# Kernel optimization log

Hardware: AMD Instinct MI355X
Metric: run time of the kernel (lower is better)

The kernel has to match this reference:

```python
import jax, jax.numpy as jnp
import numpy as np

K = 128      # knowledge_n (= net1 = prednet output width)
LOW = 64     # low_dim
PP = 64      # pp_dim
STU = 50000  # student_n
EXER = 20000 # exer_n
S_RANGES = [(0, 9999), (10000, 19999)]
NR = len(S_RANGES)
B = 4096


def setup_inputs() -> dict:
    key = jax.random.key(0)
    ks = jax.random.split(key, 16)

    def xavier(k, shape):
        fan_in, fan_out = shape[-1], shape[-2] if len(shape) > 1 else shape[-1]
        lim = np.sqrt(6.0 / (fan_in + fan_out))
        return jax.random.uniform(k, shape, jnp.float32, -lim, lim)

    return {
        "stu_id": jax.random.randint(ks[0], (B,), 0, STU),
        "exer_id": jax.random.randint(ks[1], (B,), 0, EXER),
        "kn_emb": jnp.ones((B, K), jnp.float32),
        "student_emb": xavier(ks[2], (NR, STU, LOW)),          # ParameterList stacked
        "prompt_stu": xavier(ks[3], (STU, PP)),
        "knowledge_emb": jax.random.normal(ks[4], (K, LOW), jnp.float32),
        "k_difficulty": xavier(ks[5], (EXER, LOW)),
        "s_exer_vectors": jax.random.uniform(ks[6], (NR, PP), jnp.float32),
        "W1": xavier(ks[7], (K, K + LOW)),                      # prednet_full1 (no bias)
        "W2": xavier(ks[8], (K, K + LOW)),                      # prednet_full2 (no bias)
        "W3": xavier(ks[9], (1, K)),                            # prednet_full3
        "b3": jnp.zeros((1,), jnp.float32),
        "fc1_W": xavier(ks[10], (K, PP + K)),
        "fc1_b": jnp.zeros((K,), jnp.float32),
        "fc2_W": xavier(ks[11], (K, PP + K)),
        "fc2_b": jnp.zeros((K,), jnp.float32),
    }


def reference(stu_id, exer_id, kn_emb, student_emb, prompt_stu, knowledge_emb,
              k_difficulty, s_exer_vectors, W1, W2, W3, b3, fc1_W, fc1_b, fc2_W, fc2_b):
    sig = jax.nn.sigmoid
    kle = knowledge_emb  # [K, LOW]

    # --- student side ---
    # prompt_stu.repeat(NR, 1) then index_select == index prompt_stu with stu_id % STU
    p_stu = prompt_stu[stu_id % STU]                              # [B, PP]
    stu_cat = student_emb.reshape(NR * STU, LOW)                  # concat of ParameterList
    old_stu = sig(stu_cat[stu_id] @ kle.T)                        # [B, K]
    stu_e = sig(jnp.concatenate([p_stu, old_stu], 1) @ fc1_W.T + fc1_b)  # [B, K]

    # --- exercise side ---
    counts = np.array([r[1] - r[0] + 1 for r in S_RANGES])
    temp_vectors = jnp.repeat(s_exer_vectors, counts, axis=0, total_repeat_length=EXER)
    p_exer = sig(temp_vectors[exer_id])                           # [B, PP]
    old_exer = sig(sig(k_difficulty[exer_id]) @ kle.T)            # [B, K]
    exer_e = sig(jnp.concatenate([p_exer, old_exer], 1) @ fc2_W.T + fc2_b)  # [B, K]

    # --- per-concept interaction ---
    # cat([x_broadcast, kn_vector], 2) @ W.T splits into x @ Wa.T + kle @ Wb.T
    W1a, W1b = W1[:, :K], W1[:, K:]
    W2a, W2b = W2[:, :K], W2[:, K:]
    preference = sig((stu_e @ W1a.T)[:, None, :] + (kle @ W1b.T)[None, :, :])   # [B, K, K]
    diff = sig((exer_e @ W2a.T)[:, None, :] + (kle @ W2b.T)[None, :, :])        # [B, K, K]

    o = sig((preference - diff) @ W3.T + b3)                      # [B, K, 1]
    sum_out = jnp.sum(o * kn_emb[:, :, None], axis=1)             # [B, 1]
    count = jnp.sum(kn_emb, axis=1, keepdims=True)
    return sum_out / count
```

## Files before the change

### kernel.cpp

```cpp
#include <hip/hip_runtime.h>
#include <hip/hip_bf16.h>

#define STUN   50000
#define BATCH  4096
#define LOG2E  1.4426950408889634f

__device__ __forceinline__ float fexp2(float x){ return __builtin_amdgcn_exp2f(x); }
__device__ __forceinline__ float frcp (float x){ return __builtin_amdgcn_rcpf(x); }
__device__ __forceinline__ float fsig (float x){ return frcp(1.0f + fexp2(-LOG2E * x)); }

__global__ __launch_bounds__(128) void k_pre(
    const float* __restrict__ kle,
    const float* __restrict__ W1,
    const float* __restrict__ W2,
    const float* __restrict__ fc1_W,
    const float* __restrict__ fc2_W,
    float* __restrict__ kle4,
    float* __restrict__ fc1i,
    float* __restrict__ fc2i,
    float* __restrict__ W1ai,
    float* __restrict__ W2ai,
    float* __restrict__ A1i,
    float* __restrict__ A2i)
{
    const int bid = blockIdx.x;
    const int t   = threadIdx.x;
    if (bid < 16) {
        const int u4 = bid;
        float4 v;
        v.x = kle[t * 64 + u4 * 4 + 0];
        v.y = kle[t * 64 + u4 * 4 + 1];
        v.z = kle[t * 64 + u4 * 4 + 2];
        v.w = kle[t * 64 + u4 * 4 + 3];
        *(float4*)&kle4[(u4 * 128 + t) * 4] = v;
    } else if (bid < 64) {
        const int u4 = bid - 16;
        float4 v;
        v.x = fc1_W[t * 192 + u4 * 4 + 0];
        v.y = fc1_W[t * 192 + u4 * 4 + 1];
        v.z = fc1_W[t * 192 + u4 * 4 + 2];
        v.w = fc1_W[t * 192 + u4 * 4 + 3];
        *(float4*)&fc1i[(u4 * 128 + t) * 4] = v;
    } else if (bid < 112) {
        const int u4 = bid - 64;
        float4 v;
        v.x = fc2_W[t * 192 + u4 * 4 + 0];
        v.y = fc2_W[t * 192 + u4 * 4 + 1];
        v.z = fc2_W[t * 192 + u4 * 4 + 2];
        v.w = fc2_W[t * 192 + u4 * 4 + 3];
        *(float4*)&fc2i[(u4 * 128 + t) * 4] = v;
    } else if (bid < 144) {
        const int u4 = bid - 112;
        float4 v;
        v.x = W1[t * 192 + u4 * 4 + 0];
        v.y = W1[t * 192 + u4 * 4 + 1];
        v.z = W1[t * 192 + u4 * 4 + 2];
        v.w = W1[t * 192 + u4 * 4 + 3];
        *(float4*)&W1ai[(u4 * 128 + t) * 4] = v;
    } else if (bid < 176) {
        const int u4 = bid - 144;
        float4 v;
        v.x = W2[t * 192 + u4 * 4 + 0];
        v.y = W2[t * 192 + u4 * 4 + 1];
        v.z = W2[t * 192 + u4 * 4 + 2];
        v.w = W2[t * 192 + u4 * 4 + 3];
        *(float4*)&W2ai[(u4 * 128 + t) * 4] = v;
    } else if (bid < 304) {
        const int j = bid - 176;
        float acc = 0.f;
        #pragma unroll
        for (int u4 = 0; u4 < 16; ++u4) {
            const float4 kv = *(const float4*)&kle[t * 64 + u4 * 4];
            const float4 wv = *(const float4*)&W1[j * 192 + 128 + u4 * 4];
            acc += kv.x * wv.x + kv.y * wv.y + kv.z * wv.z + kv.w * wv.w;
        }
        A1i[((j >> 2) * 128 + t) * 4 + (j & 3)] = -LOG2E * acc;
    } else {
        const int j = bid - 304;
        float acc = 0.f;
        #pragma unroll
        for (int u4 = 0; u4 < 16; ++u4) {
            const float4 kv = *(const float4*)&kle[t * 64 + u4 * 4];
            const float4 wv = *(const float4*)&W2[j * 192 + 128 + u4 * 4];
            acc += kv.x * wv.x + kv.y * wv.y + kv.z * wv.z + kv.w * wv.w;
        }
        A2i[((j >> 2) * 128 + t) * 4 + (j & 3)] = -LOG2E * acc;
    }
}

__global__ __launch_bounds__(512, 4) void k_fused(
    const int*   __restrict__ stu_id,
    const int*   __restrict__ exer_id,
    const float* __restrict__ student_emb,
    const float* __restrict__ prompt_stu,
    const float* __restrict__ k_diff,
    const float* __restrict__ s_exer,
    const float* __restrict__ kle4,
    const float* __restrict__ fc1i,
    const float* __restrict__ fc2i,
    const float* __restrict__ W1ai,
    const float* __restrict__ W2ai,
    const float* __restrict__ fc1_b,
    const float* __restrict__ fc2_b,
    const float* __restrict__ A1i,
    const float* __restrict__ A2i,
    const float* __restrict__ W3,
    const float* __restrict__ b3,
    const float* __restrict__ kn,
    float* __restrict__ out)
{
    __shared__ __align__(16) float sh_in [4][64][8];
    __shared__ __align__(16) float sh_old[2][128][8];
    __shared__ __align__(16) float sh_e  [2][128][8];
    __shared__ __align__(16) float sh_s  [2][8][128];
    __shared__ __align__(16) float ps    [2][8][128];
    __shared__ float sW3[128];
    __shared__ __align__(16) float red[8][64][4];
    __shared__ float red2_o[2][2][4];
    __shared__ float red2_k[2][2][4];

    const int t  = threadIdx.x;
    const int b0 = blockIdx.x * 8;

    {
        const int g   = t >> 6;
        const int u   = t & 63;
        const int sid = stu_id[b0 + g];
        const int eid = exer_id[b0 + g];
        const int er  = (eid >= 10000) ? 1 : 0;
        sh_in[0][u][g] = student_emb[sid * 64 + u];
        sh_in[1][u][g] = fsig(k_diff[eid * 64 + u]);
        sh_in[2][u][g] = prompt_stu[(sid % STUN) * 64 + u];
        sh_in[3][u][g] = fsig(s_exer[er * 64 + u]);
    }
    if (t < 32) *(float4*)&sW3[t * 4] = *(const float4*)&W3[t * 4];
    __syncthreads();

    const int ug   = t >> 8;
    const int tt   = t & 255;
    const int half = tt >> 7;
    const int idx  = tt & 127;

    float acc[8];

#define FMA8(xbase) { \
        const float4 x0 = *(const float4*)&(xbase)[0]; \
        const float4 x1 = *(const float4*)&(xbase)[4]; \
        acc[0] += wv * x0.x; acc[1] += wv * x0.y; acc[2] += wv * x0.z; acc[3] += wv * x0.w; \
        acc[4] += wv * x1.x; acc[5] += wv * x1.y; acc[6] += wv * x1.z; acc[7] += wv * x1.w; }

#define WSTEP(WARR, XARR, u4) { \
        const float4 w4 = *(const float4*)&WARR[((u4) * 128 + idx) * 4]; \
        { const float wv = w4.x; FMA8(XARR[(u4)*4+0]); } \
        { const float wv = w4.y; FMA8(XARR[(u4)*4+1]); } \
        { const float wv = w4.z; FMA8(XARR[(u4)*4+2]); } \
        { const float wv = w4.w; FMA8(XARR[(u4)*4+3]); } }

#define WSTEPO(WARR, XARR, u4, uoff) { \
        const float4 w4 = *(const float4*)&WARR[((u4) * 128 + idx) * 4]; \
        { const float wv = w4.x; FMA8(XARR[((u4)-(uoff))*4+0]); } \
        { const float wv = w4.y; FMA8(XARR[((u4)-(uoff))*4+1]); } \
        { const float wv = w4.z; FMA8(XARR[((u4)-(uoff))*4+2]); } \
        { const float wv = w4.w; FMA8(XARR[((u4)-(uoff))*4+3]); } }

    #pragma unroll
    for (int b = 0; b < 8; ++b) acc[b] = 0.f;
    {
        const int u4a = ug * 8;
        #pragma unroll 4
        for (int u4 = u4a; u4 < u4a + 8; ++u4) WSTEP(kle4, sh_in[half], u4);
    }
    if (ug == 1) {
        #pragma unroll
        for (int b = 0; b < 8; ++b) ps[half][b][idx] = acc[b];
    }
    __syncthreads();
    if (ug == 0) {
        #pragma unroll
        for (int b = 0; b < 8; ++b)
            sh_old[half][idx][b] = fsig(acc[b] + ps[half][b][idx]);
    }
    __syncthreads();

    #pragma unroll
    for (int b = 0; b < 8; ++b) acc[b] = 0.f;
    {
        const float* fcT = half ? fc2i : fc1i;
        if (ug == 0) {
            #pragma unroll 4
            for (int u4 = 0; u4 < 16; ++u4) WSTEP(fcT, sh_in[2 + half], u4);
            #pragma unroll 4
            for (int u4 = 16; u4 < 24; ++u4) WSTEPO(fcT, sh_old[half], u4, 16);
        } else {
            #pragma unroll 4
            for (int u4 = 24; u4 < 48; ++u4) WSTEPO(fcT, sh_old[half], u4, 16);
        }
    }
    if (ug == 1) {
        #pragma unroll
        for (int b = 0; b < 8; ++b) ps[half][b][idx] = acc[b];
    }
    __syncthreads();
    if (ug == 0) {
        const float bias = (half ? fc2_b : fc1_b)[idx];
        #pragma unroll
        for (int b = 0; b < 8; ++b)
            sh_e[half][idx][b] = fsig(acc[b] + ps[half][b][idx] + bias);
    }
    __syncthreads();

    #pragma unroll
    for (int b = 0; b < 8; ++b) acc[b] = 0.f;
    {
        const float* WT = half ? W2ai : W1ai;
        const int u4a = ug * 16;
        #pragma unroll 4
        for (int u4 = u4a; u4 < u4a + 16; ++u4) WSTEP(WT, sh_e[half], u4);
    }
    if (ug == 1) {
        #pragma unroll
        for (int b = 0; b < 8; ++b) ps[half][b][idx] = acc[b];
    }
    __syncthreads();
    if (ug == 0) {
        #pragma unroll
        for (int b = 0; b < 8; ++b)
            sh_s[half][b][idx] = -LOG2E * (acc[b] + ps[half][b][idx]);
    }
#undef FMA8
#undef WSTEP
#undef WSTEPO
    __syncthreads();

    const int w   = t >> 6;
    const int kk  = t & 63;
    const int jh  = w >> 2;
    const int kh  = (w >> 1) & 1;
    const int bq  = w & 1;
    const int k2  = kk + kh * 64;
    const int ib  = bq * 4;

    const float4* A1v = (const float4*)A1i + (jh * 16) * 128 + k2;
    const float4* A2v = (const float4*)A2i + (jh * 16) * 128 + k2;

    float ac0 = 0.f, ac1 = 0.f, ac2 = 0.f, ac3 = 0.f;

    #pragma unroll 2
    for (int j4 = 0; j4 < 16; ++j4) {
        const int j = jh * 64 + j4 * 4;
        const float4 a1 = A1v[j4 * 128];
        const float4 a2 = A2v[j4 * 128];
        const float4 w3 = *(const float4*)&sW3[j];

#define SIGPAIR(acc, s1, s2, a1c, a2c, wv) { \
        const float uu = fexp2((s1) + (a1c)); \
        const float vv = fexp2((s2) + (a2c)); \
        const float dd = frcp((1.f + uu) * (1.f + vv)); \
        acc += ((vv - uu) * dd) * (wv); }

#define BODY(acc, bi) { \
        const float4 s1 = *(const float4*)&sh_s[0][ib + bi][j]; \
        const float4 s2 = *(const float4*)&sh_s[1][ib + bi][j]; \
        SIGPAIR(acc, s1.x, s2.x, a1.x, a2.x, w3.x); \
        SIGPAIR(acc, s1.y, s2.y, a1.y, a2.y, w3.y); \
        SIGPAIR(acc, s1.z, s2.z, a1.z, a2.z, w3.z); \
        SIGPAIR(acc, s1.w, s2.w, a1.w, a2.w, w3.w); }

        BODY(ac0, 0);
        BODY(ac1, 1);
        BODY(ac2, 2);
        BODY(ac3, 3);
#undef BODY
#undef SIGPAIR
    }

    red[w][kk][0] = ac0; red[w][kk][1] = ac1;
    red[w][kk][2] = ac2; red[w][kk][3] = ac3;
    __syncthreads();
    if (w < 4) {
        const float bb3 = b3[0];
        const float4 other = *(const float4*)&red[w + 4][kk][0];
        float to[4] = { ac0 + other.x, ac1 + other.y, ac2 + other.z, ac3 + other.w };
        float co[4], ck[4];
        #pragma unroll
        for (int i = 0; i < 4; ++i) {
            const float o   = fsig(to[i] + bb3);
            const float knv = kn[(b0 + ib + i) * 128 + k2];
            co[i] = o * knv;
            ck[i] = knv;
        }
        #pragma unroll
        for (int off = 1; off < 64; off <<= 1) {
            #pragma unroll
            for (int i = 0; i < 4; ++i) {
                co[i] += __shfl_xor(co[i], off);
                ck[i] += __shfl_xor(ck[i], off);
            }
        }
        if (kk == 0) {
            #pragma unroll
            for (int i = 0; i < 4; ++i) {
                red2_o[kh][bq][i] = co[i];
                red2_k[kh][bq][i] = ck[i];
            }
        }
    }
    __syncthreads();
    if (t < 8) {
        const int b  = t;
        const int q  = b >> 2;
        const int i  = b & 3;
        const float so = red2_o[0][q][i] + red2_o[1][q][i];
        const float sk = red2_k[0][q][i] + red2_k[1][q][i];
        out[b0 + b] = so / sk;
    }
}

extern "C" void kernel_launch(void* const* d_in, const int* in_sizes, int n_in,
                              void* d_out, int out_size, void* d_ws, size_t ws_size,
                              hipStream_t stream)
{
    const int*   stu_id      = (const int*)  d_in[0];
    const int*   exer_id     = (const int*)  d_in[1];
    const float* kn_emb      = (const float*)d_in[2];
    const float* student_emb = (const float*)d_in[3];
    const float* prompt_stu  = (const float*)d_in[4];
    const float* kle         = (const float*)d_in[5];
    const float* k_diff      = (const float*)d_in[6];
    const float* s_exer      = (const float*)d_in[7];
    const float* W1          = (const float*)d_in[8];
    const float* W2          = (const float*)d_in[9];
    const float* W3          = (const float*)d_in[10];
    const float* b3          = (const float*)d_in[11];
    const float* fc1_W       = (const float*)d_in[12];
    const float* fc1_b       = (const float*)d_in[13];
    const float* fc2_W       = (const float*)d_in[14];
    const float* fc2_b       = (const float*)d_in[15];
    float* out = (float*)d_out;

    float* ws   = (float*)d_ws;
    float* kle4 = ws;
    float* fc1i = kle4 + 8192;
    float* fc2i = fc1i + 24576;
    float* W1ai = fc2i + 24576;
    float* W2ai = W1ai + 16384;
    float* A1i  = W2ai + 16384;
    float* A2i  = A1i  + 16384;

    k_pre<<<432, 128, 0, stream>>>(kle, W1, W2, fc1_W, fc2_W,
                                   kle4, fc1i, fc2i, W1ai, W2ai, A1i, A2i);
    k_fused<<<BATCH / 8, 512, 0, stream>>>(stu_id, exer_id, student_emb, prompt_stu,
                                           k_diff, s_exer, kle4, fc1i, fc2i,
                                           W1ai, W2ai, fc1_b, fc2_b,
                                           A1i, A2i, W3, b3, kn_emb, out);
}
```

Measured before the change: 53.89 us.

## Factor exp2 into precomputed exponentials and split fused kernel into prep and main

Uses exp(a+b)=exp(a)*exp(b) to precompute exponentials of the per-concept terms and of the per-sample projections, so the B×K×K inner loop needs multiplies and one reciprocal instead of two exp2 calls per element. The fused kernel is split into a prep kernel that writes per-sample exponentials to a workspace and a main kernel over 2 samples per block with 256 threads. This adds a global round trip and an extra launch, and the product form may overflow to inf for large pre-activations. The fp32 product could lose accuracy in extreme cases.

```diff
diff --git a/kernel.cpp b/kernel.cpp
--- a/kernel.cpp
+++ b/kernel.cpp
@@ -20,8 +20,8 @@
     float* __restrict__ fc2i,
     float* __restrict__ W1ai,
     float* __restrict__ W2ai,
-    float* __restrict__ A1i,
-    float* __restrict__ A2i)
+    float* __restrict__ E1i,
+    float* __restrict__ E2i)
 {
     const int bid = blockIdx.x;
     const int t   = threadIdx.x;
@@ -74,7 +74,7 @@
             const float4 wv = *(const float4*)&W1[j * 192 + 128 + u4 * 4];
             acc += kv.x * wv.x + kv.y * wv.y + kv.z * wv.z + kv.w * wv.w;
         }
-        A1i[((j >> 2) * 128 + t) * 4 + (j & 3)] = -LOG2E * acc;
+        E1i[((j >> 2) * 128 + t) * 4 + (j & 3)] = fexp2(-LOG2E * acc);
     } else {
         const int j = bid - 304;
         float acc = 0.f;
@@ -84,11 +84,11 @@
             const float4 wv = *(const float4*)&W2[j * 192 + 128 + u4 * 4];
             acc += kv.x * wv.x + kv.y * wv.y + kv.z * wv.z + kv.w * wv.w;
         }
-        A2i[((j >> 2) * 128 + t) * 4 + (j & 3)] = -LOG2E * acc;
+        E2i[((j >> 2) * 128 + t) * 4 + (j & 3)] = fexp2(-LOG2E * acc);
     }
 }
 
-__global__ __launch_bounds__(512, 4) void k_fused(
+__global__ __launch_bounds__(512, 4) void k_prep(
     const int*   __restrict__ stu_id,
     const int*   __restrict__ exer_id,
     const float* __restrict__ student_emb,
@@ -102,22 +102,13 @@
     const float* __restrict__ W2ai,
     const float* __restrict__ fc1_b,
     const float* __restrict__ fc2_b,
-    const float* __restrict__ A1i,
-    const float* __restrict__ A2i,
-    const float* __restrict__ W3,
-    const float* __restrict__ b3,
-    const float* __restrict__ kn,
-    float* __restrict__ out)
+    float* __restrict__ es1o,
+    float* __restrict__ es2o)
 {
     __shared__ __align__(16) float sh_in [4][64][8];
     __shared__ __align__(16) float sh_old[2][128][8];
     __shared__ __align__(16) float sh_e  [2][128][8];
-    __shared__ __align__(16) float sh_s  [2][8][128];
     __shared__ __align__(16) float ps    [2][8][128];
-    __shared__ float sW3[128];
-    __shared__ __align__(16) float red[8][64][4];
-    __shared__ float red2_o[2][2][4];
-    __shared__ float red2_k[2][2][4];
 
     const int t  = threadIdx.x;
     const int b0 = blockIdx.x * 8;
@@ -133,7 +124,6 @@
         sh_in[2][u][g] = prompt_stu[(sid % STUN) * 64 + u];
         sh_in[3][u][g] = fsig(s_exer[er * 64 + u]);
     }
-    if (t < 32) *(float4*)&sW3[t * 4] = *(const float4*)&W3[t * 4];
     __syncthreads();
 
     const int ug   = t >> 8;
@@ -223,96 +213,119 @@
     }
     __syncthreads();
     if (ug == 0) {
+        float* eso = half ? es2o : es1o;
         #pragma unroll
         for (int b = 0; b < 8; ++b)
-            sh_s[half][b][idx] = -LOG2E * (acc[b] + ps[half][b][idx]);
+            eso[(b0 + b) * 128 + idx] = fexp2(-LOG2E * (acc[b] + ps[half][b][idx]));
     }
 #undef FMA8
 #undef WSTEP
 #undef WSTEPO
+}
+
+__global__ __launch_bounds__(256, 6) void k_main(
+    const float* __restrict__ es1o,
+    const float* __restrict__ es2o,
+    const float* __restrict__ E1i,
+    const float* __restrict__ E2i,
+    const float* __restrict__ W3,
+    const float* __restrict__ b3,
+    const float* __restrict__ kn,
+    float* __restrict__ out)
+{
+    __shared__ __align__(16) float ses[2][2][128];
+    __shared__ float sW3[128];
+    __shared__ __align__(16) float redj[2][64][2];
+    __shared__ float red2_o[2][2];
+    __shared__ float red2_k[2][2];
+
+    const int t   = threadIdx.x;
+    const int b0  = blockIdx.x * 2;
+
+    if (t < 128) {
+        const int row  = t >> 5;
+        const int col4 = (t & 31) * 4;
+        const float* src = (row < 2) ? es1o : es2o;
+        *(float4*)&ses[row >> 1][row & 1][col4] =
+            *(const float4*)&src[(b0 + (row & 1)) * 128 + col4];
+    } else if (t < 160) {
+        const int q = t - 128;
+        *(float4*)&sW3[q * 4] = *(const float4*)&W3[q * 4];
+    }
     __syncthreads();
 
     const int w   = t >> 6;
     const int kk  = t & 63;
-    const int jh  = w >> 2;
-    const int kh  = (w >> 1) & 1;
-    const int bq  = w & 1;
-    const int k2  = kk + kh * 64;
-    const int ib  = bq * 4;
-
-    const float4* A1v = (const float4*)A1i + (jh * 16) * 128 + k2;
-    const float4* A2v = (const float4*)A2i + (jh * 16) * 128 + k2;
-
-    float ac0 = 0.f, ac1 = 0.f, ac2 = 0.f, ac3 = 0.f;
-
-    #pragma unroll 2
+    const int kh  = w & 1;
+    const int jh  = w >> 1;
+    const int k2  = kh * 64 + kk;
+
+    const float4* E1v = (const float4*)E1i;
+    const float4* E2v = (const float4*)E2i;
+
+    float acc0 = 0.f, acc1 = 0.f;
+
+#define COMP(acc, esv1, esv2, e1c, e2c, w3c) { \
+        const float uu = (esv1) * (e1c); \
+        const float vv = (esv2) * (e2c); \
+        const float dd = frcp((1.f + uu) * (1.f + vv)); \
+        acc += ((vv - uu) * dd) * (w3c); }
+
+    #pragma unroll 4
     for (int j4 = 0; j4 < 16; ++j4) {
-        const int j = jh * 64 + j4 * 4;
-        const float4 a1 = A1v[j4 * 128];
-        const float4 a2 = A2v[j4 * 128];
-        const float4 w3 = *(const float4*)&sW3[j];
-
-#define SIGPAIR(acc, s1, s2, a1c, a2c, wv) { \
-        const float uu = fexp2((s1) + (a1c)); \
-        const float vv = fexp2((s2) + (a2c)); \
-        const float dd = frcp((1.f + uu) * (1.f + vv)); \
-        acc += ((vv - uu) * dd) * (wv); }
-
-#define BODY(acc, bi) { \
-        const float4 s1 = *(const float4*)&sh_s[0][ib + bi][j]; \
-        const float4 s2 = *(const float4*)&sh_s[1][ib + bi][j]; \
-        SIGPAIR(acc, s1.x, s2.x, a1.x, a2.x, w3.x); \
-        SIGPAIR(acc, s1.y, s2.y, a1.y, a2.y, w3.y); \
-        SIGPAIR(acc, s1.z, s2.z, a1.z, a2.z, w3.z); \
-        SIGPAIR(acc, s1.w, s2.w, a1.w, a2.w, w3.w); }
-
-        BODY(ac0, 0);
-        BODY(ac1, 1);
-        BODY(ac2, 2);
-        BODY(ac3, 3);
-#undef BODY
-#undef SIGPAIR
-    }
-
-    red[w][kk][0] = ac0; red[w][kk][1] = ac1;
-    red[w][kk][2] = ac2; red[w][kk][3] = ac3;
-    __syncthreads();
-    if (w < 4) {
+        const int jj4 = jh * 16 + j4;
+        const int j   = jj4 * 4;
+        const float4 e1  = E1v[jj4 * 128 + k2];
+        const float4 e2  = E2v[jj4 * 128 + k2];
+        const float4 w3  = *(const float4*)&sW3[j];
+        const float4 s1a = *(const float4*)&ses[0][0][j];
+        const float4 s1b = *(const float4*)&ses[0][1][j];
+        const float4 s2a = *(const float4*)&ses[1][0][j];
+        const float4 s2b = *(const float4*)&ses[1][1][j];
+
+        COMP(acc0, s1a.x, s2a.x, e1.x, e2.x, w3.x);
+        COMP(acc0, s1a.y, s2a.y, e1.y, e2.y, w3.y);
+        COMP(acc0, s1a.z, s2a.z, e1.z, e2.z, w3.z);
+        COMP(acc0, s1a.w, s2a.w, e1.w, e2.w, w3.w);
+        COMP(acc1, s1b.x, s2b.x, e1.x, e2.x, w3.x);
+        COMP(acc1, s1b.y, s2b.y, e1.y, e2.y, w3.y);
+        COMP(acc1, s1b.z, s2b.z, e1.z, e2.z, w3.z);
+        COMP(acc1, s1b.w, s2b.w, e1.w, e2.w, w3.w);
+    }
+#undef COMP
+
+    if (jh == 1) {
+        redj[kh][kk][0] = acc0;
+        redj[kh][kk][1] = acc1;
+    }
+    __syncthreads();
+    if (jh == 0) {
         const float bb3 = b3[0];
-        const float4 other = *(const float4*)&red[w + 4][kk][0];
-        float to[4] = { ac0 + other.x, ac1 + other.y, ac2 + other.z, ac3 + other.w };
-        float co[4], ck[4];
-        #pragma unroll
-        for (int i = 0; i < 4; ++i) {
-            const float o   = fsig(to[i] + bb3);
-            const float knv = kn[(b0 + ib + i) * 128 + k2];
-            co[i] = o * knv;
-            ck[i] = knv;
-        }
+        const float t0 = acc0 + redj[kh][kk][0];
+        const float t1 = acc1 + redj[kh][kk][1];
+        const float o0 = fsig(t0 + bb3);
+        const float o1 = fsig(t1 + bb3);
+        const float kn0 = kn[(b0 + 0) * 128 + k2];
+        const float kn1 = kn[(b0 + 1) * 128 + k2];
+        float co0 = o0 * kn0, ck0 = kn0;
+        float co1 = o1 * kn1, ck1 = kn1;
         #pragma unroll
         for (int off = 1; off < 64; off <<= 1) {
-            #pragma unroll
-            for (int i = 0; i < 4; ++i) {
-                co[i] += __shfl_xor(co[i], off);
-                ck[i] += __shfl_xor(ck[i], off);
-            }
+            co0 += __shfl_xor(co0, off);
+            ck0 += __shfl_xor(ck0, off);
+            co1 += __shfl_xor(co1, off);
+            ck1 += __shfl_xor(ck1, off);
         }
         if (kk == 0) {
-            #pragma unroll
-            for (int i = 0; i < 4; ++i) {
-                red2_o[kh][bq][i] = co[i];
-                red2_k[kh][bq][i] = ck[i];
-            }
-        }
-    }
-    __syncthreads();
-    if (t < 8) {
-        const int b  = t;
-        const int q  = b >> 2;
-        const int i  = b & 3;
-        const float so = red2_o[0][q][i] + red2_o[1][q][i];
-        const float sk = red2_k[0][q][i] + red2_k[1][q][i];
-        out[b0 + b] = so / sk;
+            red2_o[kh][0] = co0; red2_o[kh][1] = co1;
+            red2_k[kh][0] = ck0; red2_k[kh][1] = ck1;
+        }
+    }
+    __syncthreads();
+    if (t < 2) {
+        const float so = red2_o[0][t] + red2_o[1][t];
+        const float sk = red2_k[0][t] + red2_k[1][t];
+        out[b0 + t] = so / sk;
     }
 }
 
@@ -344,13 +357,15 @@
     float* fc2i = fc1i + 24576;
     float* W1ai = fc2i + 24576;
     float* W2ai = W1ai + 16384;
-    float* A1i  = W2ai + 16384;
-    float* A2i  = A1i  + 16384;
+    float* E1i  = W2ai + 16384;
+    float* E2i  = E1i  + 16384;
+    float* es1o = E2i  + 16384;
+    float* es2o = es1o + BATCH * 128;
 
     k_pre<<<432, 128, 0, stream>>>(kle, W1, W2, fc1_W, fc2_W,
-                                   kle4, fc1i, fc2i, W1ai, W2ai, A1i, A2i);
-    k_fused<<<BATCH / 8, 512, 0, stream>>>(stu_id, exer_id, student_emb, prompt_stu,
-                                           k_diff, s_exer, kle4, fc1i, fc2i,
-                                           W1ai, W2ai, fc1_b, fc2_b,
-                                           A1i, A2i, W3, b3, kn_emb, out);
+                                   kle4, fc1i, fc2i, W1ai, W2ai, E1i, E2i);
+    k_prep<<<BATCH / 8, 512, 0, stream>>>(stu_id, exer_id, student_emb, prompt_stu,
+                                          k_diff, s_exer, kle4, fc1i, fc2i,
+                                          W1ai, W2ai, fc1_b, fc2_b, es1o, es2o);
+    k_main<<<BATCH / 2, 256, 0, stream>>>(es1o, es2o, E1i, E2i, W3, b3, kn_emb, out);
 }
```

Result: faster. 51.54 us (-4.4%).

## Factor exp of sigmoid argument into per-sample and precomputed per-concept terms

Applied to the files above, without the earlier changes.

The inner B×K×K loop previously computed exp2(s+a) for both sigmoids. It now precomputes exp(-a) for the knowledge-embedding terms in the prep kernel and exp(-s) per sample. Each pair then needs only two multiplies and one reciprocal instead of two exp2 evaluations. The block is also shrunk from 8 samples and 512 threads to 4 samples and 256 threads, which removes the split-K partial-sum exchanges in the small GEMV stages. The exp product form can overflow or underflow for large arguments, and the smaller blocks reuse each loaded weight across fewer samples.

```diff
diff --git a/kernel.cpp b/kernel.cpp
--- a/kernel.cpp
+++ b/kernel.cpp
@@ -20,8 +20,8 @@
     float* __restrict__ fc2i,
     float* __restrict__ W1ai,
     float* __restrict__ W2ai,
-    float* __restrict__ A1i,
-    float* __restrict__ A2i)
+    float* __restrict__ E1i,
+    float* __restrict__ E2i)
 {
     const int bid = blockIdx.x;
     const int t   = threadIdx.x;
@@ -74,7 +74,7 @@
             const float4 wv = *(const float4*)&W1[j * 192 + 128 + u4 * 4];
             acc += kv.x * wv.x + kv.y * wv.y + kv.z * wv.z + kv.w * wv.w;
         }
-        A1i[((j >> 2) * 128 + t) * 4 + (j & 3)] = -LOG2E * acc;
+        E1i[((j >> 2) * 128 + t) * 4 + (j & 3)] = fexp2(-LOG2E * acc);
     } else {
         const int j = bid - 304;
         float acc = 0.f;
@@ -84,11 +84,11 @@
             const float4 wv = *(const float4*)&W2[j * 192 + 128 + u4 * 4];
             acc += kv.x * wv.x + kv.y * wv.y + kv.z * wv.z + kv.w * wv.w;
         }
-        A2i[((j >> 2) * 128 + t) * 4 + (j & 3)] = -LOG2E * acc;
+        E2i[((j >> 2) * 128 + t) * 4 + (j & 3)] = fexp2(-LOG2E * acc);
     }
 }
 
-__global__ __launch_bounds__(512, 4) void k_fused(
+__global__ __launch_bounds__(256, 6) void k_fused(
     const int*   __restrict__ stu_id,
     const int*   __restrict__ exer_id,
     const float* __restrict__ student_emb,
@@ -102,25 +102,24 @@
     const float* __restrict__ W2ai,
     const float* __restrict__ fc1_b,
     const float* __restrict__ fc2_b,
-    const float* __restrict__ A1i,
-    const float* __restrict__ A2i,
+    const float* __restrict__ E1i,
+    const float* __restrict__ E2i,
     const float* __restrict__ W3,
     const float* __restrict__ b3,
     const float* __restrict__ kn,
     float* __restrict__ out)
 {
-    __shared__ __align__(16) float sh_in [4][64][8];
-    __shared__ __align__(16) float sh_old[2][128][8];
-    __shared__ __align__(16) float sh_e  [2][128][8];
-    __shared__ __align__(16) float sh_s  [2][8][128];
-    __shared__ __align__(16) float ps    [2][8][128];
+    __shared__ __align__(16) float sh_in [4][64][4];
+    __shared__ __align__(16) float sh_old[2][128][4];
+    __shared__ __align__(16) float sh_e  [2][128][4];
+    __shared__ __align__(16) float ses   [2][4][128];
     __shared__ float sW3[128];
-    __shared__ __align__(16) float red[8][64][4];
-    __shared__ float red2_o[2][2][4];
-    __shared__ float red2_k[2][2][4];
+    __shared__ __align__(16) float redj[2][64][4];
+    __shared__ float red2_o[2][4];
+    __shared__ float red2_k[2][4];
 
     const int t  = threadIdx.x;
-    const int b0 = blockIdx.x * 8;
+    const int b0 = blockIdx.x * 4;
 
     {
         const int g   = t >> 6;
@@ -136,156 +135,121 @@
     if (t < 32) *(float4*)&sW3[t * 4] = *(const float4*)&W3[t * 4];
     __syncthreads();
 
-    const int ug   = t >> 8;
-    const int tt   = t & 255;
-    const int half = tt >> 7;
-    const int idx  = tt & 127;
-
-    float acc[8];
-
-#define FMA8(xbase) { \
+    const int half = t >> 7;
+    const int idx  = t & 127;
+
+    float acc[4];
+
+#define FMA4(xbase) { \
         const float4 x0 = *(const float4*)&(xbase)[0]; \
-        const float4 x1 = *(const float4*)&(xbase)[4]; \
-        acc[0] += wv * x0.x; acc[1] += wv * x0.y; acc[2] += wv * x0.z; acc[3] += wv * x0.w; \
-        acc[4] += wv * x1.x; acc[5] += wv * x1.y; acc[6] += wv * x1.z; acc[7] += wv * x1.w; }
+        acc[0] += wv * x0.x; acc[1] += wv * x0.y; acc[2] += wv * x0.z; acc[3] += wv * x0.w; }
 
 #define WSTEP(WARR, XARR, u4) { \
         const float4 w4 = *(const float4*)&WARR[((u4) * 128 + idx) * 4]; \
-        { const float wv = w4.x; FMA8(XARR[(u4)*4+0]); } \
-        { const float wv = w4.y; FMA8(XARR[(u4)*4+1]); } \
-        { const float wv = w4.z; FMA8(XARR[(u4)*4+2]); } \
-        { const float wv = w4.w; FMA8(XARR[(u4)*4+3]); } }
+        { const float wv = w4.x; FMA4(XARR[(u4)*4+0]); } \
+        { const float wv = w4.y; FMA4(XARR[(u4)*4+1]); } \
+        { const float wv = w4.z; FMA4(XARR[(u4)*4+2]); } \
+        { const float wv = w4.w; FMA4(XARR[(u4)*4+3]); } }
 
 #define WSTEPO(WARR, XARR, u4, uoff) { \
         const float4 w4 = *(const float4*)&WARR[((u4) * 128 + idx) * 4]; \
-        { const float wv = w4.x; FMA8(XARR[((u4)-(uoff))*4+0]); } \
-        { const float wv = w4.y; FMA8(XARR[((u4)-(uoff))*4+1]); } \
-        { const float wv = w4.z; FMA8(XARR[((u4)-(uoff))*4+2]); } \
-        { const float wv = w4.w; FMA8(XARR[((u4)-(uoff))*4+3]); } }
+        { const float wv = w4.x; FMA4(XARR[((u4)-(uoff))*4+0]); } \
+        { const float wv = w4.y; FMA4(XARR[((u4)-(uoff))*4+1]); } \
+        { const float wv = w4.z; FMA4(XARR[((u4)-(uoff))*4+2]); } \
+        { const float wv = w4.w; FMA4(XARR[((u4)-(uoff))*4+3]); } }
 
     #pragma unroll
-    for (int b = 0; b < 8; ++b) acc[b] = 0.f;
-    {
-        const int u4a = ug * 8;
-        #pragma unroll 4
-        for (int u4 = u4a; u4 < u4a + 8; ++u4) WSTEP(kle4, sh_in[half], u4);
-    }
-    if (ug == 1) {
-        #pragma unroll
-        for (int b = 0; b < 8; ++b) ps[half][b][idx] = acc[b];
-    }
-    __syncthreads();
-    if (ug == 0) {
-        #pragma unroll
-        for (int b = 0; b < 8; ++b)
-            sh_old[half][idx][b] = fsig(acc[b] + ps[half][b][idx]);
-    }
-    __syncthreads();
-
+    for (int b = 0; b < 4; ++b) acc[b] = 0.f;
+    #pragma unroll 4
+    for (int u4 = 0; u4 < 16; ++u4) WSTEP(kle4, sh_in[half], u4);
     #pragma unroll
-    for (int b = 0; b < 8; ++b) acc[b] = 0.f;
+    for (int b = 0; b < 4; ++b) sh_old[half][idx][b] = fsig(acc[b]);
+    __syncthreads();
+
     {
         const float* fcT = half ? fc2i : fc1i;
-        if (ug == 0) {
-            #pragma unroll 4
-            for (int u4 = 0; u4 < 16; ++u4) WSTEP(fcT, sh_in[2 + half], u4);
-            #pragma unroll 4
-            for (int u4 = 16; u4 < 24; ++u4) WSTEPO(fcT, sh_old[half], u4, 16);
-        } else {
-            #pragma unroll 4
-            for (int u4 = 24; u4 < 48; ++u4) WSTEPO(fcT, sh_old[half], u4, 16);
-        }
-    }
-    if (ug == 1) {
-        #pragma unroll
-        for (int b = 0; b < 8; ++b) ps[half][b][idx] = acc[b];
-    }
-    __syncthreads();
-    if (ug == 0) {
+        #pragma unroll
+        for (int b = 0; b < 4; ++b) acc[b] = 0.f;
+        #pragma unroll 4
+        for (int u4 = 0; u4 < 16; ++u4) WSTEP(fcT, sh_in[2 + half], u4);
+        #pragma unroll 4
+        for (int u4 = 16; u4 < 48; ++u4) WSTEPO(fcT, sh_old[half], u4, 16);
         const float bias = (half ? fc2_b : fc1_b)[idx];
         #pragma unroll
-        for (int b = 0; b < 8; ++b)
-            sh_e[half][idx][b] = fsig(acc[b] + ps[half][b][idx] + bias);
-    }
-    __syncthreads();
-
-    #pragma unroll
-    for (int b = 0; b < 8; ++b) acc[b] = 0.f;
+        for (int b = 0; b < 4; ++b) sh_e[half][idx][b] = fsig(acc[b] + bias);
+    }
+    __syncthreads();
+
     {
         const float* WT = half ? W2ai : W1ai;
-        const int u4a = ug * 16;
+        #pragma unroll
+        for (int b = 0; b < 4; ++b) acc[b] = 0.f;
         #pragma unroll 4
-        for (int u4 = u4a; u4 < u4a + 16; ++u4) WSTEP(WT, sh_e[half], u4);
-    }
-    if (ug == 1) {
-        #pragma unroll
-        for (int b = 0; b < 8; ++b) ps[half][b][idx] = acc[b];
-    }
-    __syncthreads();
-    if (ug == 0) {
-        #pragma unroll
-        for (int b = 0; b < 8; ++b)
-            sh_s[half][b][idx] = -LOG2E * (acc[b] + ps[half][b][idx]);
-    }
-#undef FMA8
+        for (int u4 = 0; u4 < 32; ++u4) WSTEP(WT, sh_e[half], u4);
+        #pragma unroll
+        for (int b = 0; b < 4; ++b)
+            ses[half][b][idx] = fexp2(-LOG2E * acc[b]);
+    }
+#undef FMA4
 #undef WSTEP
 #undef WSTEPO
     __syncthreads();
 
     const int w   = t >> 6;
     const int kk  = t & 63;
-    const int jh  = w >> 2;
-    const int kh  = (w >> 1) & 1;
-    const int bq  = w & 1;
-    const int k2  = kk + kh * 64;
-    const int ib  = bq * 4;
-
-    const float4* A1v = (const float4*)A1i + (jh * 16) * 128 + k2;
-    const float4* A2v = (const float4*)A2i + (jh * 16) * 128 + k2;
+    const int kh  = w & 1;
+    const int jh  = w >> 1;
+    const int k2  = kh * 64 + kk;
+
+    const float4* E1v = (const float4*)E1i;
+    const float4* E2v = (const float4*)E2i;
 
     float ac0 = 0.f, ac1 = 0.f, ac2 = 0.f, ac3 = 0.f;
+
+#define COMP(acc, esv1, esv2, e1c, e2c, w3c) { \
+        const float uu = (esv1) * (e1c); \
+        const float vv = (esv2) * (e2c); \
+        const float dd = frcp((1.f + uu) * (1.f + vv)); \
+        acc += ((vv - uu) * dd) * (w3c); }
 
     #pragma unroll 2
     for (int j4 = 0; j4 < 16; ++j4) {
-        const int j = jh * 64 + j4 * 4;
-        const float4 a1 = A1v[j4 * 128];
-        const float4 a2 = A2v[j4 * 128];
+        const int jj4 = jh * 16 + j4;
+        const int j   = jj4 * 4;
+        const float4 e1 = E1v[jj4 * 128 + k2];
+        const float4 e2 = E2v[jj4 * 128 + k2];
         const float4 w3 = *(const float4*)&sW3[j];
 
-#define SIGPAIR(acc, s1, s2, a1c, a2c, wv) { \
-        const float uu = fexp2((s1) + (a1c)); \
-        const float vv = fexp2((s2) + (a2c)); \
-        const float dd = frcp((1.f + uu) * (1.f + vv)); \
-        acc += ((vv - uu) * dd) * (wv); }
-
 #define BODY(acc, bi) { \
-        const float4 s1 = *(const float4*)&sh_s[0][ib + bi][j]; \
-        const float4 s2 = *(const float4*)&sh_s[1][ib + bi][j]; \
-        SIGPAIR(acc, s1.x, s2.x, a1.x, a2.x, w3.x); \
-        SIGPAIR(acc, s1.y, s2.y, a1.y, a2.y, w3.y); \
-        SIGPAIR(acc, s1.z, s2.z, a1.z, a2.z, w3.z); \
-        SIGPAIR(acc, s1.w, s2.w, a1.w, a2.w, w3.w); }
+        const float4 s1 = *(const float4*)&ses[0][bi][j]; \
+        const float4 s2 = *(const float4*)&ses[1][bi][j]; \
+        COMP(acc, s1.x, s2.x, e1.x, e2.x, w3.x); \
+        COMP(acc, s1.y, s2.y, e1.y, e2.y, w3.y); \
+        COMP(acc, s1.z, s2.z, e1.z, e2.z, w3.z); \
+        COMP(acc, s1.w, s2.w, e1.w, e2.w, w3.w); }
 
         BODY(ac0, 0);
         BODY(ac1, 1);
         BODY(ac2, 2);
         BODY(ac3, 3);
 #undef BODY
-#undef SIGPAIR
-    }
-
-    red[w][kk][0] = ac0; red[w][kk][1] = ac1;
-    red[w][kk][2] = ac2; red[w][kk][3] = ac3;
-    __syncthreads();
-    if (w < 4) {
+    }
+#undef COMP
+
+    if (jh == 1) {
+        redj[kh][kk][0] = ac0; redj[kh][kk][1] = ac1;
+        redj[kh][kk][2] = ac2; redj[kh][kk][3] = ac3;
+    }
+    __syncthreads();
+    if (jh == 0) {
         const float bb3 = b3[0];
-        const float4 other = *(const float4*)&red[w + 4][kk][0];
+        const float4 other = *(const float4*)&redj[kh][kk][0];
         float to[4] = { ac0 + other.x, ac1 + other.y, ac2 + other.z, ac3 + other.w };
         float co[4], ck[4];
         #pragma unroll
         for (int i = 0; i < 4; ++i) {
             const float o   = fsig(to[i] + bb3);
-            const float knv = kn[(b0 + ib + i) * 128 + k2];
+            const float knv = kn[(b0 + i) * 128 + k2];
             co[i] = o * knv;
             ck[i] = knv;
         }
@@ -300,19 +264,16 @@
         if (kk == 0) {
             #pragma unroll
             for (int i = 0; i < 4; ++i) {
-                red2_o[kh][bq][i] = co[i];
-                red2_k[kh][bq][i] = ck[i];
+                red2_o[kh][i] = co[i];
+                red2_k[kh][i] = ck[i];
             }
         }
     }
     __syncthreads();
-    if (t < 8) {
-        const int b  = t;
-        const int q  = b >> 2;
-        const int i  = b & 3;
-        const float so = red2_o[0][q][i] + red2_o[1][q][i];
-        const float sk = red2_k[0][q][i] + red2_k[1][q][i];
-        out[b0 + b] = so / sk;
+    if (t < 4) {
+        const float so = red2_o[0][t] + red2_o[1][t];
+        const float sk = red2_k[0][t] + red2_k[1][t];
+        out[b0 + t] = so / sk;
     }
 }
 
@@ -344,13 +305,13 @@
     float* fc2i = fc1i + 24576;
     float* W1ai = fc2i + 24576;
     float* W2ai = W1ai + 16384;
-    float* A1i  = W2ai + 16384;
-    float* A2i  = A1i  + 16384;
+    float* E1i  = W2ai + 16384;
+    float* E2i  = E1i  + 16384;
 
     k_pre<<<432, 128, 0, stream>>>(kle, W1, W2, fc1_W, fc2_W,
-                                   kle4, fc1i, fc2i, W1ai, W2ai, A1i, A2i);
-    k_fused<<<BATCH / 8, 512, 0, stream>>>(stu_id, exer_id, student_emb, prompt_stu,
+                                   kle4, fc1i, fc2i, W1ai, W2ai, E1i, E2i);
+    k_fused<<<BATCH / 4, 256, 0, stream>>>(stu_id, exer_id, student_emb, prompt_stu,
                                            k_diff, s_exer, kle4, fc1i, fc2i,
                                            W1ai, W2ai, fc1_b, fc2_b,
-                                           A1i, A2i, W3, b3, kn_emb, out);
+                                           E1i, E2i, W3, b3, kn_emb, out);
 }
```

Result: slower. 55.13 us (+2.3%).
